# Kernel tuning notes

Measured on AMD Instinct MI355X. Metric: run time of the kernel, lower is better.

The kernel has to match this reference:

```python
import jax, jax.numpy as jnp
import numpy as np

EPS = 1e-6  # mmdet bbox_overlaps eps


def _nearest_bev(boxes7):
    # boxes7: [N, 7] = (x, y, z, dx, dy, dz, yaw). LiDARInstance3DBoxes.nearest_bev:
    # limit yaw to [-pi/2, pi/2) via limit_period(yaw, 0.5, pi); if |yaw| > pi/4 swap dx/dy,
    # then return axis-aligned (x1, y1, x2, y2).
    x, y = boxes7[:, 0], boxes7[:, 1]
    dx, dy = boxes7[:, 3], boxes7[:, 4]
    yaw = boxes7[:, 6]
    pi = jnp.float32(np.pi)
    normed = jnp.abs(yaw - jnp.floor(yaw / pi + 0.5) * pi)
    swap = normed > pi / 4
    w = jnp.where(swap, dy, dx)
    h = jnp.where(swap, dx, dy)
    return jnp.stack([x - w / 2, y - h / 2, x + w / 2, y + h / 2], axis=-1)


def _pairwise_iou(b):
    # b: [N, 4] x1y1x2y2 -> [N, N] IoU (mmdet bbox_overlaps, mode='iou')
    area = (b[:, 2] - b[:, 0]) * (b[:, 3] - b[:, 1])
    lt = jnp.maximum(b[:, None, :2], b[None, :, :2])
    rb = jnp.minimum(b[:, None, 2:], b[None, :, 2:])
    wh = jnp.clip(rb - lt, 0.0)
    inter = wh[..., 0] * wh[..., 1]
    union = jnp.maximum(area[:, None] + area[None, :] - inter, EPS)
    return inter / union


def setup_inputs() -> dict:
    key = jax.random.key(0)
    k1, k2, k3, k4, k5, k6 = jax.random.split(key, 6)
    B, A, C, H, W, box_dim = 2, 2, 10, 32, 32, 7
    N = H * W * A
    scores = jax.random.normal(k1, (B, A * C, H, W), jnp.float32)
    bbox_preds = jax.random.normal(k2, (B, A * box_dim, H, W), jnp.float32)
    pp_params = jax.random.normal(k3, (B, C * 3, H, W), jnp.float32)
    centers = jax.random.uniform(k4, (B, N, 3), jnp.float32, 0.0, 50.0)
    sizes = jax.random.uniform(k5, (B, N, 3), jnp.float32, 1.0, 5.0)
    yaw = jax.random.uniform(k6, (B, N, 1), jnp.float32, -np.pi, np.pi)
    decoded = jnp.concatenate([centers, sizes, yaw], axis=-1)  # [B, N, 7]
    return {"scores": scores, "bbox_preds": bbox_preds, "pp_params": pp_params, "decoded": decoded}


def reference(scores, bbox_preds, pp_params, decoded):
    B, AC, H, W = scores.shape
    N = decoded.shape[1]
    A = N // (H * W)
    C = AC // A
    # flatten_scores: (B,A,C,H,W) -> (B,H,W,A,C) -> (B, HWA, C)
    sc_f = scores.reshape(B, A, C, H, W).transpose(0, 3, 4, 1, 2).reshape(B, N, C)
    # flatten_pp: (B,C,3,H,W) -> (B,H,W,C,3), broadcast over A -> (B, HWA, C, 3)
    pp_hw = pp_params.reshape(B, C, 3, H, W).transpose(0, 3, 4, 1, 2)  # [B,H,W,C,3]
    pp_f = jnp.broadcast_to(pp_hw[:, :, :, None, :, :], (B, H, W, A, C, 3)).reshape(B, N, C, 3)
    # per-batch BEV IoU matrices
    bev = jax.vmap(_nearest_bev)(decoded[..., :7])        # [B, N, 4]
    iou = jax.vmap(_pairwise_iou)(bev)                    # [B, N, N]
    # per-class outer-product bias + row softmax + matmul with column softmax of scores
    p0 = pp_f[..., 0]                                     # [B, N, C]
    p1 = pp_f[..., 1]                                     # [B, N, C]
    bias = p0[:, :, None, :] * p1[:, None, :, :]          # [B, N, N, C]
    weight = jax.nn.softmax(iou[..., None] + bias, axis=2)  # softmax over keys (dim=1 of NxN)
    sm_sc = jax.nn.softmax(sc_f, axis=1)                  # softmax over N per class
    new_sc = jnp.einsum('bnmc,bmc->bnc', weight, sm_sc)   # [B, N, C]
    # un-flatten back to level layout: (B,H,W,A,C) -> (B, A*C, H, W)
    out_scores = new_sc.reshape(B, H, W, A, C).transpose(0, 3, 4, 1, 2).reshape(B, A * C, H, W)
    return out_scores, bbox_preds, pp_params
```

## Files before the change

### kernel.cpp

```cpp
#include <hip/hip_runtime.h>
#include <math.h>

#define Bz 2
#define Az 2
#define Cz 10
#define HWz 1024
#define Nz 2048
#define ACHW (Az*Cz*HWz)
#define NBBOX (Bz*Az*7*HWz)
#define NPP   (Bz*Cz*3*HWz)
#define EPSf 1e-6f
#define LOG2E 1.4426950408889634f

#if __has_builtin(__builtin_amdgcn_exp2f)
#define EXP2F(x) __builtin_amdgcn_exp2f(x)
#else
#define EXP2F(x) exp2f(x)
#endif
#if __has_builtin(__builtin_amdgcn_rcpf)
#define RCPF(x) __builtin_amdgcn_rcpf(x)
#else
#define RCPF(x) (1.0f/(x))
#endif


__global__ __launch_bounds__(256) void k_pre(const float* __restrict__ scores,
                                             const float* __restrict__ bbox,
                                             const float* __restrict__ pp,
                                             const float* __restrict__ dec,
                                             float* __restrict__ out,
                                             float2* __restrict__ LT,
                                             float2* __restrict__ RB,
                                             float2* __restrict__ PQ) {
    int blk = blockIdx.x;
    int tid = threadIdx.x;
    __shared__ float red[256];

    if (blk < 240) {
        int i = blk * 256 + tid;
        if (i < NBBOX) out[Bz*ACHW + i] = bbox[i];
        if (i < NPP)   out[Bz*ACHW + NBBOX + i] = pp[i];
        return;
    }
    if (blk < 256) {
        int i = (blk - 240) * 256 + tid;
        const float* d = dec + i*7;
        float x = d[0], y = d[1], dx = d[3], dy = d[4], yaw = d[6];
        const float PI = 3.14159265358979323846f;
        float normed = fabsf(yaw - floorf(yaw/PI + 0.5f) * PI);
        bool swp = normed > PI * 0.25f;
        float w = swp ? dy : dx;
        float h = swp ? dx : dy;
        LT[i] = make_float2(x - 0.5f*w, y - 0.5f*h);
        RB[i] = make_float2(x + 0.5f*w, y + 0.5f*h);
        return;
    }
    int bc = blk - 256;
    int b = bc / Cz, c = bc % Cz;
    const float* sbase = scores + b*ACHW;
    float vals[Nz/256];
    float mx = -INFINITY;
    #pragma unroll
    for (int j = 0; j < Nz/256; j++) {
        int n = tid + j*256;
        int a = n & 1, hw = n >> 1;
        float v = sbase[(a*Cz + c)*HWz + hw];
        vals[j] = v;
        mx = fmaxf(mx, v);
    }
    red[tid] = mx; __syncthreads();
    for (int s = 128; s > 0; s >>= 1) {
        if (tid < s) red[tid] = fmaxf(red[tid], red[tid+s]);
        __syncthreads();
    }
    mx = red[0]; __syncthreads();
    float sum = 0.f;
    #pragma unroll
    for (int j = 0; j < Nz/256; j++) {
        vals[j] = EXP2F((vals[j] - mx) * LOG2E);
        sum += vals[j];
    }
    red[tid] = sum; __syncthreads();
    for (int s = 128; s > 0; s >>= 1) {
        if (tid < s) red[tid] += red[tid+s];
        __syncthreads();
    }
    float inv = 1.f / red[0];
    const float* p1base = pp + b*Cz*3*HWz + (c*3 + 1)*HWz;
    #pragma unroll
    for (int j = 0; j < Nz/256; j++) {
        int n = tid + j*256;
        int hw = n >> 1;
        PQ[(b*Cz + c)*Nz + n] = make_float2(p1base[hw] * LOG2E, vals[j] * inv);
    }
}

__global__ __launch_bounds__(256, 4) void k_main(const float2* __restrict__ LT,
                                                 const float2* __restrict__ RB,
                                                 const float2* __restrict__ PQ,
                                                 const float* __restrict__ pp,
                                                 float* __restrict__ out) {
    __shared__ float4 S4[1536];
    float2* Sf2 = (float2*)S4;
    int tid = threadIdx.x;
    int wave = tid >> 6, lane = tid & 63;
    int row = blockIdx.x * 4 + wave;
    int b = row / Nz, n = row % Nz;
    int hw = n >> 1, a = n & 1;

    float2 ltn = LT[row], rbn = RB[row];
    float area_n = (rbn.x - ltn.x) * (rbn.y - ltn.y);

    float p0[Cz];
    const float* p0base = pp + b*Cz*3*HWz + hw;
    #pragma unroll
    for (int c = 0; c < Cz; c++) p0[c] = p0base[c*3*HWz];

    float l[Cz], acc[Cz];
    #pragma unroll
    for (int c = 0; c < Cz; c++) { l[c] = 0.f; acc[c] = 0.f; }

    const float4* LT4b = (const float4*)(LT + b*Nz);
    const float4* RB4b = (const float4*)(RB + b*Nz);
    const float4* PQ4b = (const float4*)(PQ + b*Cz*Nz);

    for (int chunk = 0; chunk < Nz/256; chunk++) {
        int f40 = chunk * 128;
        __syncthreads();
        #pragma unroll
        for (int k = 0; k < 6; k++) {
            int u = tid + k*256;
            float4 v;
            if (u < 128)       v = LT4b[f40 + u];
            else if (u < 256)  v = RB4b[f40 + (u - 128)];
            else {
                int w2 = u - 256;
                int c = w2 >> 7, i = w2 & 127;
                v = PQ4b[c*(Nz/2) + f40 + i];
            }
            S4[u] = v;
        }
        __syncthreads();
        #pragma unroll
        for (int k2 = 0; k2 < 4; k2++) {
            int m = lane + (k2 << 6);
            float2 bl = Sf2[m];
            float2 br = Sf2[256 + m];
            float xx1 = fmaxf(ltn.x, bl.x), yy1 = fmaxf(ltn.y, bl.y);
            float xx2 = fminf(rbn.x, br.x), yy2 = fminf(rbn.y, br.y);
            float iw = fmaxf(xx2 - xx1, 0.f), ih = fmaxf(yy2 - yy1, 0.f);
            float inter = iw * ih;
            float am = (br.x - bl.x) * (br.y - bl.y);
            float uni = fmaxf(area_n + am - inter, EPSf);
            float iou2 = inter * LOG2E * RCPF(uni);
            #pragma unroll
            for (int c = 0; c < Cz; c++) {
                float2 pq = Sf2[512 + c*256 + m];
                float e = EXP2F(fmaf(p0[c], pq.x, iou2));
                l[c] += e;
                acc[c] = fmaf(e, pq.y, acc[c]);
            }
        }
    }

    #pragma unroll
    for (int c = 0; c < Cz; c++) {
        for (int off = 32; off > 0; off >>= 1) {
            l[c]   += __shfl_down(l[c], off);
            acc[c] += __shfl_down(acc[c], off);
        }
    }
    if (lane == 0) {
        #pragma unroll
        for (int c = 0; c < Cz; c++)
            out[b*ACHW + (a*Cz + c)*HWz + hw] = acc[c] / l[c];
    }
}

extern "C" void kernel_launch(void* const* d_in, const int* in_sizes, int n_in,
                              void* d_out, int out_size, void* d_ws, size_t ws_size,
                              hipStream_t stream) {
    const float* scores = (const float*)d_in[0];
    const float* bbox   = (const float*)d_in[1];
    const float* pp     = (const float*)d_in[2];
    const float* dec    = (const float*)d_in[3];
    float* out = (float*)d_out;

    float2* LT = (float2*)d_ws;
    float2* RB = LT + (size_t)Bz*Nz;
    float2* PQ = RB + (size_t)Bz*Nz;

    hipLaunchKernelGGL(k_pre,  dim3(276),  dim3(256), 0, stream,
                       scores, bbox, pp, dec, out, LT, RB, PQ);
    hipLaunchKernelGGL(k_main, dim3(Bz*Nz/4), dim3(256), 0, stream,
                       LT, RB, PQ, pp, out);
}
```

Measured before the change: 90.58 us.

## Factor exp(iou+bias) into separable terms exploiting shared p1 across anchors

Splits exp2(iou + p0*p1) into exp2(iou) times exp2(p0*p1), and uses the fact that p0/p1 are shared between the two anchors at each spatial location. Each wave now handles both anchors of one hw position and iterates over hw keys, so exp count drops from N*N*C to roughly (4 + C) per pair of key cells. It also packs the softmaxed scores as bf16, software-pipelines global loads into registers ahead of shared-memory stores, and uses DPP wave reductions. The bf16 packing lowers precision of the score weights, and the factored exponent may overflow for large biases.

```diff
diff --git a/kernel.cpp b/kernel.cpp
--- a/kernel.cpp
+++ b/kernel.cpp
@@ -23,6 +23,48 @@
 #define RCPF(x) (1.0f/(x))
 #endif
 
+static __device__ __forceinline__ unsigned short f2bf(float x) {
+    unsigned u = __builtin_bit_cast(unsigned, x);
+    unsigned r = (u + 0x7fffu + ((u >> 16) & 1u)) >> 16;
+    return (unsigned short)r;
+}
+
+#if __has_builtin(__builtin_amdgcn_update_dpp)
+static __device__ __forceinline__ float wred(float x) {
+    int t;
+    t = __builtin_amdgcn_update_dpp(0, __builtin_bit_cast(int, x), 0x111, 0xf, 0xf, true);
+    x += __builtin_bit_cast(float, t);
+    t = __builtin_amdgcn_update_dpp(0, __builtin_bit_cast(int, x), 0x112, 0xf, 0xf, true);
+    x += __builtin_bit_cast(float, t);
+    t = __builtin_amdgcn_update_dpp(0, __builtin_bit_cast(int, x), 0x114, 0xf, 0xf, true);
+    x += __builtin_bit_cast(float, t);
+    t = __builtin_amdgcn_update_dpp(0, __builtin_bit_cast(int, x), 0x118, 0xf, 0xf, true);
+    x += __builtin_bit_cast(float, t);
+    t = __builtin_amdgcn_update_dpp(0, __builtin_bit_cast(int, x), 0x142, 0xa, 0xf, true);
+    x += __builtin_bit_cast(float, t);
+    t = __builtin_amdgcn_update_dpp(0, __builtin_bit_cast(int, x), 0x143, 0xc, 0xf, true);
+    x += __builtin_bit_cast(float, t);
+    return x;
+}
+#define WRED_LANE 63
+#else
+static __device__ __forceinline__ float wred(float x) {
+    for (int off = 32; off > 0; off >>= 1) x += __shfl_down(x, off);
+    return x;
+}
+#define WRED_LANE 0
+#endif
+
+static __device__ __forceinline__ float iou_e(float nx1,float ny1,float nx2,float ny2,float ar,
+                                              float mx1,float my1,float mx2,float my2,float am) {
+    float xx1 = fmaxf(nx1, mx1), yy1 = fmaxf(ny1, my1);
+    float xx2 = fminf(nx2, mx2), yy2 = fminf(ny2, my2);
+    float iw = fmaxf(xx2 - xx1, 0.f), ih = fmaxf(yy2 - yy1, 0.f);
+    float inter = iw * ih;
+    float uni = fmaxf(ar + am - inter, EPSf);
+    return EXP2F(inter * LOG2E * RCPF(uni));
+}
+
 
 __global__ __launch_bounds__(256) void k_pre(const float* __restrict__ scores,
                                              const float* __restrict__ bbox,
@@ -31,7 +73,7 @@
                                              float* __restrict__ out,
                                              float2* __restrict__ LT,
                                              float2* __restrict__ RB,
-                                             float2* __restrict__ PQ) {
+                                             uint2* __restrict__ GPQ) {
     int blk = blockIdx.x;
     int tid = threadIdx.x;
     __shared__ float red[256];
@@ -87,93 +129,117 @@
     }
     float inv = 1.f / red[0];
     const float* p1base = pp + b*Cz*3*HWz + (c*3 + 1)*HWz;
+    uint2* gp = GPQ + (b*Cz + c)*HWz;
     #pragma unroll
     for (int j = 0; j < Nz/256; j++) {
-        int n = tid + j*256;
-        int hw = n >> 1;
-        PQ[(b*Cz + c)*Nz + n] = make_float2(p1base[hw] * LOG2E, vals[j] * inv);
-    }
-}
-
-__global__ __launch_bounds__(256, 4) void k_main(const float2* __restrict__ LT,
-                                                 const float2* __restrict__ RB,
-                                                 const float2* __restrict__ PQ,
-                                                 const float* __restrict__ pp,
-                                                 float* __restrict__ out) {
-    __shared__ float4 S4[1536];
-    float2* Sf2 = (float2*)S4;
+        __syncthreads();
+        red[tid] = vals[j] * inv;
+        __syncthreads();
+        if (tid < 128) {
+            int hm = (j << 7) + tid;
+            float q0 = red[2*tid], q1 = red[2*tid + 1];
+            unsigned qq = (unsigned)f2bf(q0) | ((unsigned)f2bf(q1) << 16);
+            float p1 = p1base[hm] * LOG2E;
+            gp[hm] = make_uint2(__builtin_bit_cast(unsigned, p1), qq);
+        }
+    }
+}
+
+__global__ __launch_bounds__(256) void k_main(const float4* __restrict__ LT4,
+                                              const float4* __restrict__ RB4,
+                                              const uint2* __restrict__ GPQ,
+                                              const float* __restrict__ pp,
+                                              float* __restrict__ out) {
+    __shared__ float4 SB[256];
+    __shared__ uint2  SPQ[Cz*128];
     int tid = threadIdx.x;
     int wave = tid >> 6, lane = tid & 63;
-    int row = blockIdx.x * 4 + wave;
-    int b = row / Nz, n = row % Nz;
-    int hw = n >> 1, a = n & 1;
-
-    float2 ltn = LT[row], rbn = RB[row];
-    float area_n = (rbn.x - ltn.x) * (rbn.y - ltn.y);
+    int bid = blockIdx.x;
+    int b = bid >> 8;
+    int hn = ((bid & 255) << 2) + wave;
+
+    const float4* LTb = LT4 + (b << 10);
+    const float4* RBb = RB4 + (b << 10);
+    const uint2*  PQb = GPQ + b * (Cz * HWz);
+
+    float4 bx = LTb[hn];
+    float4 by = RBb[hn];
+    float ar0 = (by.x - bx.x) * (by.y - bx.y);
+    float ar1 = (by.z - bx.z) * (by.w - bx.w);
 
     float p0[Cz];
-    const float* p0base = pp + b*Cz*3*HWz + hw;
-    #pragma unroll
-    for (int c = 0; c < Cz; c++) p0[c] = p0base[c*3*HWz];
-
-    float l[Cz], acc[Cz];
-    #pragma unroll
-    for (int c = 0; c < Cz; c++) { l[c] = 0.f; acc[c] = 0.f; }
-
-    const float4* LT4b = (const float4*)(LT + b*Nz);
-    const float4* RB4b = (const float4*)(RB + b*Nz);
-    const float4* PQ4b = (const float4*)(PQ + b*Cz*Nz);
-
-    for (int chunk = 0; chunk < Nz/256; chunk++) {
-        int f40 = chunk * 128;
-        __syncthreads();
+    const float* p0base = pp + b*(Cz*3*HWz) + hn;
+    #pragma unroll
+    for (int c = 0; c < Cz; c++) p0[c] = p0base[c * 3 * HWz];
+
+    float l0[Cz], l1[Cz], a0[Cz], a1[Cz];
+    #pragma unroll
+    for (int c = 0; c < Cz; c++) { l0[c]=0.f; l1[c]=0.f; a0[c]=0.f; a1[c]=0.f; }
+
+    float4 rB = (tid < 128) ? LTb[tid] : RBb[tid - 128];
+    uint2 rq[5];
+    #pragma unroll
+    for (int k = 0; k < 5; k++) {
+        int u = tid + (k << 8);
+        rq[k] = PQb[((u >> 7) << 10) + (u & 127)];
+    }
+
+    for (int cb = 0; cb < 8; cb++) {
+        __syncthreads();
+        SB[tid] = rB;
         #pragma unroll
-        for (int k = 0; k < 6; k++) {
-            int u = tid + k*256;
-            float4 v;
-            if (u < 128)       v = LT4b[f40 + u];
-            else if (u < 256)  v = RB4b[f40 + (u - 128)];
-            else {
-                int w2 = u - 256;
-                int c = w2 >> 7, i = w2 & 127;
-                v = PQ4b[c*(Nz/2) + f40 + i];
+        for (int k = 0; k < 5; k++) SPQ[tid + (k << 8)] = rq[k];
+        __syncthreads();
+        if (cb < 7) {
+            int nb = (cb + 1) << 7;
+            rB = (tid < 128) ? LTb[nb + tid] : RBb[nb + tid - 128];
+            #pragma unroll
+            for (int k = 0; k < 5; k++) {
+                int u = tid + (k << 8);
+                rq[k] = PQb[((u >> 7) << 10) + nb + (u & 127)];
             }
-            S4[u] = v;
-        }
-        __syncthreads();
+        }
         #pragma unroll
-        for (int k2 = 0; k2 < 4; k2++) {
-            int m = lane + (k2 << 6);
-            float2 bl = Sf2[m];
-            float2 br = Sf2[256 + m];
-            float xx1 = fmaxf(ltn.x, bl.x), yy1 = fmaxf(ltn.y, bl.y);
-            float xx2 = fminf(rbn.x, br.x), yy2 = fminf(rbn.y, br.y);
-            float iw = fmaxf(xx2 - xx1, 0.f), ih = fmaxf(yy2 - yy1, 0.f);
-            float inter = iw * ih;
-            float am = (br.x - bl.x) * (br.y - bl.y);
-            float uni = fmaxf(area_n + am - inter, EPSf);
-            float iou2 = inter * LOG2E * RCPF(uni);
+        for (int half = 0; half < 2; half++) {
+            int hm = (half << 6) + lane;
+            float4 bl = SB[hm];
+            float4 br = SB[128 + hm];
+            float am0 = (br.x - bl.x) * (br.y - bl.y);
+            float am1 = (br.z - bl.z) * (br.w - bl.w);
+            float E00 = iou_e(bx.x,bx.y,by.x,by.y,ar0, bl.x,bl.y,br.x,br.y,am0);
+            float E01 = iou_e(bx.x,bx.y,by.x,by.y,ar0, bl.z,bl.w,br.z,br.w,am1);
+            float E10 = iou_e(bx.z,bx.w,by.z,by.w,ar1, bl.x,bl.y,br.x,br.y,am0);
+            float E11 = iou_e(bx.z,bx.w,by.z,by.w,ar1, bl.z,bl.w,br.z,br.w,am1);
+            float S0 = E00 + E01, S1 = E10 + E11;
             #pragma unroll
             for (int c = 0; c < Cz; c++) {
-                float2 pq = Sf2[512 + c*256 + m];
-                float e = EXP2F(fmaf(p0[c], pq.x, iou2));
-                l[c] += e;
-                acc[c] = fmaf(e, pq.y, acc[c]);
+                uint2 pq = SPQ[(c << 7) + hm];
+                float p1 = __builtin_bit_cast(float, pq.x);
+                float q0 = __builtin_bit_cast(float, pq.y << 16);
+                float q1 = __builtin_bit_cast(float, pq.y & 0xffff0000u);
+                float F = EXP2F(p0[c] * p1);
+                l0[c] = fmaf(F, S0, l0[c]);
+                l1[c] = fmaf(F, S1, l1[c]);
+                float t0 = fmaf(E01, q1, E00 * q0);
+                float t1 = fmaf(E11, q1, E10 * q0);
+                a0[c] = fmaf(F, t0, a0[c]);
+                a1[c] = fmaf(F, t1, a1[c]);
             }
         }
     }
 
     #pragma unroll
     for (int c = 0; c < Cz; c++) {
-        for (int off = 32; off > 0; off >>= 1) {
-            l[c]   += __shfl_down(l[c], off);
-            acc[c] += __shfl_down(acc[c], off);
-        }
-    }
-    if (lane == 0) {
+        l0[c] = wred(l0[c]); l1[c] = wred(l1[c]);
+        a0[c] = wred(a0[c]); a1[c] = wred(a1[c]);
+    }
+    if (lane == WRED_LANE) {
+        float* ob = out + b*ACHW + hn;
         #pragma unroll
-        for (int c = 0; c < Cz; c++)
-            out[b*ACHW + (a*Cz + c)*HWz + hw] = acc[c] / l[c];
+        for (int c = 0; c < Cz; c++) {
+            ob[c * HWz]        = a0[c] * RCPF(l0[c]);
+            ob[(Cz + c) * HWz] = a1[c] * RCPF(l1[c]);
+        }
     }
 }
 
@@ -188,10 +254,10 @@
 
     float2* LT = (float2*)d_ws;
     float2* RB = LT + (size_t)Bz*Nz;
-    float2* PQ = RB + (size_t)Bz*Nz;
-
-    hipLaunchKernelGGL(k_pre,  dim3(276),  dim3(256), 0, stream,
+    uint2*  PQ = (uint2*)(RB + (size_t)Bz*Nz);
+
+    hipLaunchKernelGGL(k_pre,  dim3(276), dim3(256), 0, stream,
                        scores, bbox, pp, dec, out, LT, RB, PQ);
-    hipLaunchKernelGGL(k_main, dim3(Bz*Nz/4), dim3(256), 0, stream,
-                       LT, RB, PQ, pp, out);
-}
+    hipLaunchKernelGGL(k_main, dim3(512), dim3(256), 0, stream,
+                       (const float4*)LT, (const float4*)RB, PQ, pp, out);
+}
```

After: 81.41 us. 1.11x faster.
